# Optimization experiments

Measured on AMD Instinct MI355X. Metric: run time of the kernel, lower is better.

The kernel has to match this reference:

```python
import jax, jax.numpy as jnp
import numpy as np

# dims
L, E, D, DFF, H = 4, 4, 512, 2048, 8
B, T, S, K = 16, 256, 512, 2
HD = D // H


def _ln(x, g, b, eps=1e-5):
    m = x.mean(-1, keepdims=True)
    v = ((x - m) ** 2).mean(-1, keepdims=True)
    return (x - m) / jnp.sqrt(v + eps) * g + b


def _mha(xq, xkv, in_w, in_b, out_w, out_b):
    # torch nn.MultiheadAttention (batch_first), no masks, eval mode
    qw, kw, vw = jnp.split(in_w, 3, axis=0)
    qb, kb, vb = jnp.split(in_b, 3)
    q = xq @ qw.T + qb                       # [B,T,D]
    k = xkv @ kw.T + kb                      # [B,S,D]
    v = xkv @ vw.T + vb
    def heads(t):
        b, s, _ = t.shape
        return t.reshape(b, s, H, HD).transpose(0, 2, 1, 3)
    q, k, v = heads(q), heads(k), heads(v)   # [B,H,*,HD]
    scale = 1.0 / float(np.sqrt(HD))
    a = jax.nn.softmax(jnp.einsum('bhtd,bhsd->bhts', q, k) * scale, axis=-1)
    o = jnp.einsum('bhts,bhsd->bhtd', a, v)
    o = o.transpose(0, 2, 1, 3).reshape(xq.shape[0], xq.shape[1], D)
    return o @ out_w.T + out_b


def _expert(p, x, mem):
    (siw, sib, sow, sob, ciw, cib, cow, cob,
     l1w, l1b, l2w, l2b, g1, b1, g2, b2, g3, b3) = p
    sa = _mha(x, x, siw, sib, sow, sob)
    x = _ln(x + sa, g1, b1)
    ca = _mha(x, mem, ciw, cib, cow, cob)
    x = _ln(x + ca, g2, b2)
    ffn = jax.nn.relu(x @ l1w.T + l1b) @ l2w.T + l2b
    x = _ln(x + ffn, g3, b3)
    return x


def _forward(tgt, memory, router_w, params):
    x = tgt
    for l in range(L):
        pooled = x.mean(axis=1)                      # [B,D] sample-level routing
        logits = pooled @ router_w[l].T              # [B,E]
        vals, idx = jax.lax.top_k(logits, K)
        w = jax.nn.softmax(vals.astype(jnp.float32), axis=-1).astype(x.dtype)
        # dense [B,E] combine weights: zero for unselected experts -> same math
        wf = jnp.zeros((x.shape[0], E), x.dtype).at[jnp.arange(x.shape[0])[:, None], idx].add(w)
        p_l = jax.tree_util.tree_map(lambda a: a[l], params)   # each [E,...]
        outs = jax.vmap(_expert, in_axes=(0, None, None))(p_l, x, memory)  # [E,B,T,D]
        x = jnp.einsum('be,ebtd->btd', wf, outs)
    return x


def setup_inputs() -> dict:
    key = jax.random.key(0)
    ks = jax.random.split(key, 16)
    n = lambda k, shape: jax.random.normal(k, shape, jnp.float32) * 0.02
    return {
        'tgt': jax.random.normal(ks[0], (B, T, D), jnp.float32),
        'memory': jax.random.normal(ks[1], (B, S, D), jnp.float32),
        'router_w': n(ks[2], (L, E, D)),
        'sa_in_w': n(ks[3], (L, E, 3 * D, D)), 'sa_in_b': jnp.zeros((L, E, 3 * D)),
        'sa_out_w': n(ks[4], (L, E, D, D)), 'sa_out_b': jnp.zeros((L, E, D)),
        'ca_in_w': n(ks[5], (L, E, 3 * D, D)), 'ca_in_b': jnp.zeros((L, E, 3 * D)),
        'ca_out_w': n(ks[6], (L, E, D, D)), 'ca_out_b': jnp.zeros((L, E, D)),
        'lin1_w': n(ks[7], (L, E, DFF, D)), 'lin1_b': jnp.zeros((L, E, DFF)),
        'lin2_w': n(ks[8], (L, E, D, DFF)), 'lin2_b': jnp.zeros((L, E, D)),
        'n1_g': jnp.ones((L, E, D)), 'n1_b': jnp.zeros((L, E, D)),
        'n2_g': jnp.ones((L, E, D)), 'n2_b': jnp.zeros((L, E, D)),
        'n3_g': jnp.ones((L, E, D)), 'n3_b': jnp.zeros((L, E, D)),
    }


def reference(tgt, memory, router_w, sa_in_w, sa_in_b, sa_out_w, sa_out_b,
              ca_in_w, ca_in_b, ca_out_w, ca_out_b, lin1_w, lin1_b, lin2_w, lin2_b,
              n1_g, n1_b, n2_g, n2_b, n3_g, n3_b):
    params = (sa_in_w, sa_in_b, sa_out_w, sa_out_b, ca_in_w, ca_in_b, ca_out_w, ca_out_b,
              lin1_w, lin1_b, lin2_w, lin2_b, n1_g, n1_b, n2_g, n2_b, n3_g, n3_b)
    return _forward(tgt, memory, router_w, params)
```

## Files before the change

kernel.cpp:

```cpp
#include <hip/hip_runtime.h>
#include <hip/hip_bf16.h>

#define L_ 4
#define E_ 4
#define D_ 512
#define DFF_ 2048
#define H_ 8
#define B_ 16
#define T_ 256
#define S_ 512
#define HD_ 64
#define NSLOT 32

typedef __attribute__((ext_vector_type(4))) float f32x4;
typedef __attribute__((ext_vector_type(8))) short bf16x8;
typedef __attribute__((ext_vector_type(4))) int i32x4;

static __device__ __forceinline__ float bf2f(unsigned short u){
  union{float f; unsigned u;} c; c.u = ((unsigned)u)<<16; return c.f;
}
static __device__ __forceinline__ unsigned short f2bf(float f){
  union{float f; unsigned u;} c; c.f=f;
  unsigned u=c.u;
  return (unsigned short)((u + 0x7FFFu + ((u>>16)&1u))>>16);
}

static __device__ __forceinline__ void gload16(const unsigned short* g, unsigned short* l){
  __builtin_amdgcn_global_load_lds(
      (const __attribute__((address_space(1))) void*)g,
      (__attribute__((address_space(3))) void*)l, 16, 0, 0);
}

static __device__ __forceinline__ int xcd_swz(int orig, int nwg){
  int q = nwg >> 3, r = nwg & 7;
  int xcd = orig & 7, idx = orig >> 3;
  return (xcd < r) ? (xcd*(q+1) + idx) : (r*(q+1) + (xcd-r)*q + idx);
}

__global__ void __launch_bounds__(256) route_k(const float* __restrict__ x,
    const float* __restrict__ rw, int* __restrict__ eidx, float* __restrict__ wgt)
{
  __shared__ float pooled[D_];
  __shared__ float logit[E_];
  int b = blockIdx.x, tid = threadIdx.x;
  for (int d = tid; d < D_; d += 256) {
    float s = 0.f;
    const float* xp = x + ((long)b*T_)*D_ + d;
    for (int t=0;t<T_;t++) s += xp[(long)t*D_];
    pooled[d] = s * (1.f/T_);
  }
  __syncthreads();
  int wave = tid>>6, lane = tid&63;
  {
    float s=0.f;
    const float* w = rw + (long)wave*D_;
    for (int d=lane; d<D_; d+=64) s += pooled[d]*w[d];
    #pragma unroll
    for (int o=32;o;o>>=1) s += __shfl_xor(s,o);
    if (lane==0) logit[wave] = s;
  }
  __syncthreads();
  if (tid==0){
    int i1=0; float v1=logit[0];
    for (int e=1;e<E_;e++) if (logit[e] > v1){ v1=logit[e]; i1=e; }
    int i2=-1; float v2=-3.4e38f;
    for (int e=0;e<E_;e++) if (e!=i1 && logit[e] > v2){ v2=logit[e]; i2=e; }
    float e2 = __expf(v2 - v1);
    float w1 = 1.f/(1.f+e2);
    eidx[2*b]=i1; eidx[2*b+1]=i2;
    wgt[2*b]=w1; wgt[2*b+1]=e2*w1;
  }
}

__global__ void __launch_bounds__(256) cast_bf16_k(const float* __restrict__ in,
    unsigned short* __restrict__ out, long n){
  long i = ((long)blockIdx.x*blockDim.x + threadIdx.x)*4;
  long st = (long)gridDim.x*blockDim.x*4;
  for (; i<n; i+=st){
    float4 v = *(const float4*)(in+i);
    ushort4 o; o.x=f2bf(v.x); o.y=f2bf(v.y); o.z=f2bf(v.z); o.w=f2bf(v.w);
    *(ushort4*)(out+i) = o;
  }
}

__global__ void __launch_bounds__(256) cast_weights_k(
    const float* __restrict__ s0, const float* __restrict__ s1,
    const float* __restrict__ s2, const float* __restrict__ s3,
    const float* __restrict__ s4, const float* __restrict__ s5,
    unsigned short* __restrict__ d0, unsigned short* __restrict__ d1,
    unsigned short* __restrict__ d2, unsigned short* __restrict__ d3,
    unsigned short* __restrict__ d4, unsigned short* __restrict__ d5)
{
  const long N0=(long)E_*3*D_*D_, N1=(long)E_*D_*D_;
  const long N2=N0, N3=N1, N4=(long)E_*DFF_*D_, N5=N4;
  const long total = N0+N1+N2+N3+N4+N5;
  long i = ((long)blockIdx.x*256 + threadIdx.x)*4;
  long st = (long)gridDim.x*256*4;
  for (; i<total; i+=st){
    const float* s; unsigned short* d; long j = i;
    if (j < N0){ s=s0; d=d0; }
    else if ((j-=N0) < N1){ s=s1; d=d1; }
    else if ((j-=N1) < N2){ s=s2; d=d2; }
    else if ((j-=N2) < N3){ s=s3; d=d3; }
    else if ((j-=N3) < N4){ s=s4; d=d4; }
    else { j-=N4; s=s5; d=d5; }
    float4 v = *(const float4*)(s+j);
    ushort4 o; o.x=f2bf(v.x); o.y=f2bf(v.y); o.z=f2bf(v.z); o.w=f2bf(v.w);
    *(ushort4*)(d+j) = o;
  }
}

__global__ void __launch_bounds__(256) vtrans_k(const unsigned short* __restrict__ src,
    long sSlot, int ld, unsigned short* __restrict__ dst, int rows)
{
  __shared__ unsigned short t[64][68];
  int s0 = blockIdx.x*64; int h = blockIdx.y; int slot = blockIdx.z;
  const unsigned short* sp = src + (long)slot*sSlot + (long)h*64;
  int c = threadIdx.x&63, w = threadIdx.x>>6;
  #pragma unroll
  for (int i=0;i<16;i++){
    int r = i*4 + w;
    t[r][c] = sp[(long)(s0+r)*ld + c];
  }
  __syncthreads();
  unsigned short* dp = dst + ((long)slot*H_ + h)*((long)64*rows) + s0;
  #pragma unroll
  for (int i=0;i<16;i++){
    int d = i*4 + w;
    dp[(long)d*rows + c] = t[c][d];
  }
}

template<int NT>
__global__ void __launch_bounds__(256) fattn_k(
    const unsigned short* __restrict__ Qg, long qSlot, int ldq,
    const unsigned short* __restrict__ Kg, long kSlot, int ldk,
    const unsigned short* __restrict__ Vtg,
    unsigned short* __restrict__ Og, long oSlot, int ldo)
{
  constexpr int SLEN = NT*64;
  __shared__ unsigned short K_lds[64][72];
  __shared__ unsigned short V_lds[64][72];
  __shared__ unsigned short P_lds[4][16][72];

  int nwg = gridDim.x*gridDim.y;
  int wg = xcd_swz(blockIdx.x + gridDim.x*blockIdx.y, nwg);
  int qb = wg % gridDim.x;
  int z  = wg / gridDim.x;
  int slot = z >> 3, h = z & 7;
  int tid = threadIdx.x, wave = tid>>6, lane = tid&63;
  int lr = lane&15, lg = lane>>4;
  int lk = lg*8;

  const unsigned short* Qp = Qg + (long)slot*qSlot + (long)h*HD_;
  const unsigned short* Kp = Kg + (long)slot*kSlot + (long)h*HD_;
  const unsigned short* Vp = Vtg + (long)z*((long)HD_*SLEN);

  bf16x8 qf[2];
  {
    int qrow = qb*64 + wave*16 + lr;
    const unsigned short* qr = Qp + (long)qrow*ldq;
    qf[0] = *(const bf16x8*)(qr + lk);
    qf[1] = *(const bf16x8*)(qr + 32 + lk);
  }

  float m_prev[4], l_run[4];
  f32x4 acc_o[4];
  #pragma unroll
  for (int r=0;r<4;r++){ m_prev[r]=-1e30f; l_run[r]=0.f; }
  #pragma unroll
  for (int ni=0;ni<4;ni++) acc_o[ni]=(f32x4){0.f,0.f,0.f,0.f};

  int srow = tid>>3, sch = tid&7;

  i32x4 kr0 = *(const i32x4*)(Kp + (long)srow*ldk + sch*8);
  i32x4 kr1 = *(const i32x4*)(Kp + (long)(srow+32)*ldk + sch*8);
  i32x4 vr0 = *(const i32x4*)(Vp + (long)srow*SLEN + sch*8);
  i32x4 vr1 = *(const i32x4*)(Vp + (long)(srow+32)*SLEN + sch*8);

  for (int t=0; t<NT; ++t){
    __syncthreads();
    *(i32x4*)&K_lds[srow][sch*8] = kr0;
    *(i32x4*)&K_lds[srow+32][sch*8] = kr1;
    *(i32x4*)&V_lds[srow][sch*8] = vr0;
    *(i32x4*)&V_lds[srow+32][sch*8] = vr1;
    __syncthreads();

    int tn = (t+1 < NT) ? t+1 : t;
    int k0n = tn*64;
    kr0 = *(const i32x4*)(Kp + (long)(k0n+srow)*ldk + sch*8);
    kr1 = *(const i32x4*)(Kp + (long)(k0n+srow+32)*ldk + sch*8);
    vr0 = *(const i32x4*)(Vp + (long)srow*SLEN + k0n + sch*8);
    vr1 = *(const i32x4*)(Vp + (long)(srow+32)*SLEN + k0n + sch*8);

    f32x4 s[4];
    #pragma unroll
    for (int ni=0;ni<4;ni++) s[ni]=(f32x4){0.f,0.f,0.f,0.f};
    __builtin_amdgcn_s_setprio(1);
    #pragma unroll
    for (int ki=0;ki<2;ki++){
      #pragma unroll
      for (int ni=0;ni<4;ni++){
        bf16x8 kf = *(const bf16x8*)&K_lds[ni*16+lr][ki*32+lk];
        s[ni] = __builtin_amdgcn_mfma_f32_16x16x32_bf16(qf[ki], kf, s[ni],0,0,0);
      }
    }
    __builtin_amdgcn_s_setprio(0);
    float tmax[4];
    #pragma unroll
    for (int r=0;r<4;r++){
      tmax[r] = fmaxf(fmaxf(s[0][r],s[1][r]),fmaxf(s[2][r],s[3][r]));
      #pragma unroll
      for (int msk=1; msk<16; msk<<=1) tmax[r]=fmaxf(tmax[r], __shfl_xor(tmax[r],msk));
    }
    bool inc = (tmax[0]>m_prev[0])|(tmax[1]>m_prev[1])|(tmax[2]>m_prev[2])|(tmax[3]>m_prev[3]);
    if (__any(inc)){
      #pragma unroll
      for (int r=0;r<4;r++){
        float mnew = fmaxf(m_prev[r], tmax[r]);
        float corr = __expf(m_prev[r]-mnew);
        m_prev[r] = mnew;
        l_run[r] *= corr;
        #pragma unroll
        for (int ni=0;ni<4;ni++) acc_o[ni][r] *= corr;
      }
    }
    float rs[4] = {0.f,0.f,0.f,0.f};
    #pragma unroll
    for (int ni=0;ni<4;ni++){
      #pragma unroll
      for (int r=0;r<4;r++){
        float p = __expf(s[ni][r]-m_prev[r]);
        rs[r] += p;
        P_lds[wave][lg*4+r][ni*16+lr] = f2bf(p);
      }
    }
    #pragma unroll
    for (int r=0;r<4;r++){
      #pragma unroll
      for (int msk=1; msk<16; msk<<=1) rs[r] += __shfl_xor(rs[r],msk);
      l_run[r] += rs[r];
    }
    __builtin_amdgcn_s_setprio(1);
    #pragma unroll
    for (int ki=0;ki<2;ki++){
      bf16x8 pf = *(const bf16x8*)&P_lds[wave][lr][ki*32+lk];
      #pragma unroll
      for (int ni=0;ni<4;ni++){
        bf16x8 vf = *(const bf16x8*)&V_lds[ni*16+lr][ki*32+lk];
        acc_o[ni] = __builtin_amdgcn_mfma_f32_16x16x32_bf16(pf, vf, acc_o[ni],0,0,0);
      }
    }
    __builtin_amdgcn_s_setprio(0);
  }
  unsigned short* Op = Og + (long)slot*oSlot + (long)h*HD_;
  #pragma unroll
  for (int r=0;r<4;r++){
    float inv = 1.f/l_run[r];
    int q = qb*64 + wave*16 + lg*4 + r;
    #pragma unroll
    for (int ni=0;ni<4;ni++)
      Op[(long)q*ldo + ni*16 + lr] = f2bf(acc_o[ni][r]*inv);
  }
}

template<int BM, int BN, int WTM, int WTN, int BK>
__global__ void __launch_bounds__(512) gemm_lds(
    const unsigned short* __restrict__ A, long aSlot, int aDiv, long aHead, int lda,
    const unsigned short* __restrict__ W, long wSlot, long wHead, long wExp, int ldw,
    const int* __restrict__ eidx, const float* __restrict__ bias, long biasExp,
    void* __restrict__ Cp, long cSlot, long cHead, int ldc,
    int K, int HZ, int f32out, int relu, int scaleNlim, float scaleVal)
{
  constexpr int WAVES_N = BN/WTN;
  constexpr int MI = WTM/16, NI = WTN/16;
  constexpr int SLOTS = BK/8;
  static_assert((BM/WTM)*(BN/WTN) == 8, "8 waves");
  static_assert((BM*SLOTS)%512==0 && (BN*SLOTS)%512==0, "stage coverage");
  __shared__ unsigned short smem[2*(BM+BN)*BK];

  int nwg = gridDim.x*gridDim.y*gridDim.z;
  int wg = xcd_swz(blockIdx.x + gridDim.x*(blockIdx.y + gridDim.y*blockIdx.z), nwg);
  int bx = wg % gridDim.x; int t1 = wg / gridDim.x;
  int by = t1 % gridDim.y; int z  = t1 / gridDim.y;

  int slot = z / HZ;
  int h = z - slot*HZ;
  int e = eidx ? eidx[slot] : 0;
  const unsigned short* Ap = A + (long)(slot/aDiv)*aSlot + (long)h*aHead;
  const unsigned short* Wp = W + (long)slot*wSlot + (long)h*wHead + (long)e*wExp;
  const float* bp = bias ? (bias + (long)e*biasExp) : nullptr;

  int tid  = threadIdx.x;
  int wave = tid>>6, lane = tid&63;
  int wm = wave / WAVES_N, wn = wave % WAVES_N;
  int bm0 = by*BM;
  int bn0 = bx*BN;
  int lr = lane&15;
  int lg = lane>>4;
  int swz = (BK==64) ? (lr&7) : ((lr>>1)&3);

  Ap += (long)bm0*lda;
  Wp += (long)bn0*ldw;

  f32x4 acc[MI][NI];
  #pragma unroll
  for (int i=0;i<MI;i++)
  #pragma unroll
  for (int j=0;j<NI;j++) acc[i][j] = (f32x4){0.f,0.f,0.f,0.f};

  auto stage = [&](int buf, int k0){
    unsigned short* as = &smem[(size_t)buf*(BM+BN)*BK];
    unsigned short* bs = as + BM*BK;
    #pragma unroll
    for (int i=0;i<BM*SLOTS/512;i++){
      int cch = i*512 + tid;
      int row = cch / SLOTS, c = cch % SLOTS;
      int cs = (BK==64) ? (c ^ (row&7)) : (c ^ ((row>>1)&3));
      gload16(Ap + (long)row*lda + k0 + (cs<<3), as + cch*8);
    }
    #pragma unroll
    for (int i=0;i<BN*SLOTS/512;i++){
      int cch = i*512 + tid;
      int row = cch / SLOTS, c = cch % SLOTS;
      int cs = (BK==64) ? (c ^ (row&7)) : (c ^ ((row>>1)&3));
      gload16(Wp + (long)row*ldw + k0 + (cs<<3), bs + cch*8);
    }
  };

  auto compute = [&](int buf){
    unsigned short* as = &smem[(size_t)buf*(BM+BN)*BK];
    unsigned short* bs = as + BM*BK;
    #pragma unroll
    for (int ki=0;ki<BK/32;ki++){
      bf16x8 af[MI], bfr[NI];
      #pragma unroll
      for (int mi=0;mi<MI;mi++){
        int row = wm*WTM + mi*16 + lr;
        af[mi] = *(const bf16x8*)&as[row*BK + (((ki*4+lg) ^ swz)<<3)];
      }
      #pragma unroll
      for (int ni=0;ni<NI;ni++){
        int row = wn*WTN + ni*16 + lr;
        bfr[ni] = *(const bf16x8*)&bs[row*BK + (((ki*4+lg) ^ swz)<<3)];
      }
      __builtin_amdgcn_s_setprio(1);
      #pragma unroll
      for (int mi=0;mi<MI;mi++)
      #pragma unroll
      for (int ni=0;ni<NI;ni++)
        acc[mi][ni] = __builtin_amdgcn_mfma_f32_16x16x32_bf16(af[mi], bfr[ni], acc[mi][ni], 0,0,0);
      __builtin_amdgcn_s_setprio(0);
    }
  };

  int NT = K / BK;
  stage(0, 0);
  __syncthreads();
  int cur = 0;
  for (int t=0; t<NT; ++t){
    if (t+1 < NT) stage(cur^1, (t+1)*BK);
    compute(cur);
    __syncthreads();
    cur ^= 1;
  }

  long cbase = (long)slot*cSlot + (long)h*cHead;
  int rbase = lg*4;
  #pragma unroll
  for (int mi=0;mi<MI;mi++)
  #pragma unroll
  for (int ni=0;ni<NI;ni++){
    f32x4 v = acc[mi][ni];
    int n = bn0 + wn*WTN + ni*16 + lr;
    float bv = bp ? bp[n] : 0.f;
    float scv = (n < scaleNlim) ? scaleVal : 1.f;
    #pragma unroll
    for (int r=0;r<4;r++){
      int m = bm0 + wm*WTM + mi*16 + rbase + r;
      float val = (v[r] + bv) * scv;
      if (relu) val = fmaxf(val, 0.f);
      long o = cbase + (long)m*ldc + n;
      if (f32out) ((float*)Cp)[o] = val;
      else ((unsigned short*)Cp)[o] = f2bf(val);
    }
  }
}

__global__ void __launch_bounds__(256) add_ln_k(
    const float* __restrict__ Ab, int aDiv, long aStride,
    const unsigned short* __restrict__ Bb, long bStride,
    const float* __restrict__ G, const float* __restrict__ Bt,
    const int* __restrict__ eidx,
    float* __restrict__ OutF, unsigned short* __restrict__ OutB)
{
  int row = blockIdx.x*4 + (threadIdx.x>>6);
  int slot = row>>8, t = row&255;
  int lane = threadIdx.x&63;
  const float* a = Ab + (long)(slot/aDiv)*aStride + (long)t*D_;
  const unsigned short* b = Bb + (long)slot*bStride + (long)t*D_;
  int e = eidx[slot];
  const float* g  = G  + (long)e*D_;
  const float* bt = Bt + (long)e*D_;
  float x[8]; float s=0.f;
  #pragma unroll
  for (int i=0;i<8;i++){ x[i] = a[lane+i*64]+bf2f(b[lane+i*64]); s+=x[i]; }
  #pragma unroll
  for (int o=32;o;o>>=1) s += __shfl_xor(s,o);
  float m = s*(1.f/D_);
  float q=0.f;
  #pragma unroll
  for (int i=0;i<8;i++){ float d=x[i]-m; q+=d*d; }
  #pragma unroll
  for (int o=32;o;o>>=1) q += __shfl_xor(q,o);
  float rs = rsqrtf(q*(1.f/D_)+1e-5f);
  long ob = (long)slot*(T_*D_) + (long)t*D_;
  #pragma unroll
  for (int i=0;i<8;i++){
    int d = lane+i*64;
    float y = (x[i]-m)*rs*g[d]+bt[d];
    OutF[ob+d]=y;
    if (OutB) OutB[ob+d]=f2bf(y);
  }
}

__global__ void __launch_bounds__(256) add_ln_comb_k(
    const float* __restrict__ x2, const unsigned short* __restrict__ proj,
    const float* __restrict__ G, const float* __restrict__ Bt,
    const int* __restrict__ eidx, const float* __restrict__ wgt,
    float* __restrict__ dstF, unsigned short* __restrict__ dstB)
{
  int row = blockIdx.x*4 + (threadIdx.x>>6);
  int b = row>>8, t = row&255;
  int lane = threadIdx.x&63;
  float out[8];
  #pragma unroll
  for (int i=0;i<8;i++) out[i]=0.f;
  #pragma unroll
  for (int s2i=0;s2i<2;s2i++){
    int slot = 2*b + s2i;
    int e = eidx[slot];
    float w = wgt[slot];
    const float* a = x2 + (long)slot*(T_*D_) + (long)t*D_;
    const unsigned short* p = proj + (long)slot*(T_*D_) + (long)t*D_;
    const float* g  = G  + (long)e*D_;
    const float* bt = Bt + (long)e*D_;
    float x[8]; float s=0.f;
    #pragma unroll
    for (int i=0;i<8;i++){ x[i] = a[lane+i*64]+bf2f(p[lane+i*64]); s+=x[i]; }
    #pragma unroll
    for (int o=32;o;o>>=1) s += __shfl_xor(s,o);
    float m = s*(1.f/D_);
    float q=0.f;
    #pragma unroll
    for (int i=0;i<8;i++){ float d=x[i]-m; q+=d*d; }
    #pragma unroll
    for (int o=32;o;o>>=1) q += __shfl_xor(q,o);
    float rs = rsqrtf(q*(1.f/D_)+1e-5f);
    #pragma unroll
    for (int i=0;i<8;i++){
      int d = lane+i*64;
      out[i] += w*((x[i]-m)*rs*g[d]+bt[d]);
    }
  }
  long ob = (long)row*D_;
  #pragma unroll
  for (int i=0;i<8;i++){
    int d = lane+i*64;
    dstF[ob+d] = out[i];
    dstB[ob+d] = f2bf(out[i]);
  }
}

extern "C" void kernel_launch(void* const* d_in, const int* in_sizes, int n_in,
                              void* d_out, int out_size, void* d_ws, size_t ws_size,
                              hipStream_t stream)
{
  const float* tgt      = (const float*)d_in[0];
  const float* memory   = (const float*)d_in[1];
  const float* router_w = (const float*)d_in[2];
  const float* sa_in_w  = (const float*)d_in[3];
  const float* sa_in_b  = (const float*)d_in[4];
  const float* sa_out_w = (const float*)d_in[5];
  const float* sa_out_b = (const float*)d_in[6];
  const float* ca_in_w  = (const float*)d_in[7];
  const float* ca_in_b  = (const float*)d_in[8];
  const float* ca_out_w = (const float*)d_in[9];
  const float* ca_out_b = (const float*)d_in[10];
  const float* lin1_w   = (const float*)d_in[11];
  const float* lin1_b   = (const float*)d_in[12];
  const float* lin2_w   = (const float*)d_in[13];
  const float* lin2_b   = (const float*)d_in[14];
  const float* n1_g = (const float*)d_in[15];
  const float* n1_b = (const float*)d_in[16];
  const float* n2_g = (const float*)d_in[17];
  const float* n2_b = (const float*)d_in[18];
  const float* n3_g = (const float*)d_in[19];
  const float* n3_b = (const float*)d_in[20];

  char* ws = (char*)d_ws;
  size_t off = 0;
  auto alloc = [&](size_t bytes)->char*{
    char* p = ws + off; off += (bytes + 255) & ~(size_t)255; return p;
  };
  unsigned short* xb    = (unsigned short*)alloc(2ull*B_*T_*D_);
  unsigned short* memb  = (unsigned short*)alloc(2ull*B_*S_*D_);
  float*          x     = (float*)alloc(4ull*B_*T_*D_);
  int*            eidx  = (int*)alloc(4ull*NSLOT);
  float*          wgt   = (float*)alloc(4ull*NSLOT);
  unsigned short* wSaIn  = (unsigned short*)alloc(2ull*E_*3*D_*D_);
  unsigned short* wSaOut = (unsigned short*)alloc(2ull*E_*D_*D_);
  unsigned short* wCaIn  = (unsigned short*)alloc(2ull*E_*3*D_*D_);
  unsigned short* wCaOut = (unsigned short*)alloc(2ull*E_*D_*D_);
  unsigned short* wL1    = (unsigned short*)alloc(2ull*E_*DFF_*D_);
  unsigned short* wL2    = (unsigned short*)alloc(2ull*E_*D_*DFF_);
  unsigned short* qkv   = (unsigned short*)alloc(2ull*NSLOT*T_*3*D_);
  unsigned short* ffh   = (unsigned short*)alloc(2ull*NSLOT*T_*DFF_);
  unsigned short* attn  = (unsigned short*)alloc(2ull*NSLOT*T_*D_);
  unsigned short* proj  = (unsigned short*)alloc(2ull*NSLOT*T_*D_);
  float*          x1    = (float*)alloc(4ull*NSLOT*T_*D_);
  unsigned short* x1b   = (unsigned short*)alloc(2ull*NSLOT*T_*D_);
  unsigned short* cq    = (unsigned short*)alloc(2ull*NSLOT*T_*D_);
  unsigned short* mkv   = (unsigned short*)alloc(2ull*NSLOT*S_*2*D_);
  float*          x2    = (float*)alloc(4ull*NSLOT*T_*D_);
  unsigned short* x2b   = (unsigned short*)alloc(2ull*NSLOT*T_*D_);
  unsigned short* Vt1   = cq;
  unsigned short* Vt2   = qkv;

  cast_bf16_k<<<1024,256,0,stream>>>(tgt,    xb,   (long)B_*T_*D_);
  cast_bf16_k<<<1024,256,0,stream>>>(memory, memb, (long)B_*S_*D_);

  const float* xcur = tgt;
  for (int l=0; l<L_; ++l){
    route_k<<<B_,256,0,stream>>>(xcur, router_w + (size_t)l*E_*D_, eidx, wgt);
    cast_weights_k<<<2048,256,0,stream>>>(
      sa_in_w  + (size_t)l*E_*3*D_*D_, sa_out_w + (size_t)l*E_*D_*D_,
      ca_in_w  + (size_t)l*E_*3*D_*D_, ca_out_w + (size_t)l*E_*D_*D_,
      lin1_w   + (size_t)l*E_*DFF_*D_, lin2_w   + (size_t)l*E_*D_*DFF_,
      wSaIn, wSaOut, wCaIn, wCaOut, wL1, wL2);

    gemm_lds<128,256,64,64,32><<<dim3(6,2,NSLOT),512,0,stream>>>(
      xb, (long)T_*D_, 2, 0, D_,
      wSaIn, 0, 0, (long)3*D_*D_, D_,
      eidx, sa_in_b + (size_t)l*E_*3*D_, 3*D_,
      qkv, (long)T_*3*D_, 0, 3*D_,
      512, 1, 0, 0, D_, 0.125f);
    vtrans_k<<<dim3(T_/64,H_,NSLOT),256,0,stream>>>(
      qkv + 2*D_, (long)T_*3*D_, 3*D_, Vt1, T_);
    fattn_k<4><<<dim3(T_/64, NSLOT*H_),256,0,stream>>>(
      qkv, (long)T_*3*D_, 3*D_,
      qkv + D_, (long)T_*3*D_, 3*D_,
      Vt1, attn, (long)T_*D_, D_);
    gemm_lds<128,128,64,32,64><<<dim3(4,2,NSLOT),512,0,stream>>>(
      attn, (long)T_*D_, 1, 0, D_,
      wSaOut, 0, 0, (long)D_*D_, D_,
      eidx, sa_out_b + (size_t)l*E_*D_, D_,
      proj, (long)T_*D_, 0, D_,
      512, 1, 0, 0, 0, 1.f);
    add_ln_k<<<2048,256,0,stream>>>(xcur, 2, (long)T_*D_, proj, (long)T_*D_,
      n1_g + (size_t)l*E_*D_, n1_b + (size_t)l*E_*D_, eidx, x1, x1b);
    gemm_lds<128,128,64,32,64><<<dim3(4,2,NSLOT),512,0,stream>>>(
      x1b, (long)T_*D_, 1, 0, D_,
      wCaIn, 0, 0, (long)3*D_*D_, D_,
      eidx, ca_in_b + (size_t)l*E_*3*D_, 3*D_,
      cq, (long)T_*D_, 0, D_,
      512, 1, 0, 0, D_, 0.125f);
    gemm_lds<128,256,64,64,32><<<dim3(4,4,NSLOT),512,0,stream>>>(
      memb, (long)S_*D_, 2, 0, D_,
      wCaIn + (size_t)D_*D_, 0, 0, (long)3*D_*D_, D_,
      eidx, ca_in_b + (size_t)l*E_*3*D_ + D_, 3*D_,
      mkv, (long)S_*2*D_, 0, 2*D_,
      512, 1, 0, 0, 0, 1.f);
    vtrans_k<<<dim3(S_/64,H_,NSLOT),256,0,stream>>>(
      mkv + D_, (long)S_*2*D_, 2*D_, Vt2, S_);
    fattn_k<8><<<dim3(T_/64, NSLOT*H_),256,0,stream>>>(
      cq, (long)T_*D_, D_,
      mkv, (long)S_*2*D_, 2*D_,
      Vt2, attn, (long)T_*D_, D_);
    gemm_lds<128,128,64,32,64><<<dim3(4,2,NSLOT),512,0,stream>>>(
      attn, (long)T_*D_, 1, 0, D_,
      wCaOut, 0, 0, (long)D_*D_, D_,
      eidx, ca_out_b + (size_t)l*E_*D_, D_,
      proj, (long)T_*D_, 0, D_,
      512, 1, 0, 0, 0, 1.f);
    add_ln_k<<<2048,256,0,stream>>>(x1, 1, (long)T_*D_, proj, (long)T_*D_,
      n2_g + (size_t)l*E_*D_, n2_b + (size_t)l*E_*D_, eidx, x2, x2b);
    gemm_lds<128,256,64,64,32><<<dim3(8,2,NSLOT),512,0,stream>>>(
      x2b, (long)T_*D_, 1, 0, D_,
      wL1, 0, 0, (long)DFF_*D_, D_,
      eidx, lin1_b + (size_t)l*E_*DFF_, DFF_,
      ffh, (long)T_*DFF_, 0, DFF_,
      512, 1, 0, 1, 0, 1.f);
    gemm_lds<128,128,64,32,64><<<dim3(4,2,NSLOT),512,0,stream>>>(
      ffh, (long)T_*DFF_, 1, 0, DFF_,
      wL2, 0, 0, (long)D_*DFF_, DFF_,
      eidx, lin2_b + (size_t)l*E_*D_, D_,
      proj, (long)T_*D_, 0, D_,
      2048, 1, 0, 0, 0, 1.f);
    float* dstF = (l==L_-1) ? (float*)d_out : x;
    add_ln_comb_k<<<1024,256,0,stream>>>(x2, proj,
      n3_g + (size_t)l*E_*D_, n3_b + (size_t)l*E_*D_, eidx, wgt, dstF, xb);
    xcur = x;
  }
}
```

Before: 1.081 ms.

## Parallelize routing pool, drop fp32 residual copies, vectorize layernorm kernels

```diff
diff --git a/kernel.cpp b/kernel.cpp
--- a/kernel.cpp
+++ b/kernel.cpp
@@ -37,16 +37,32 @@
   return (xcd < r) ? (xcd*(q+1) + idx) : (r*(q+1) + (xcd-r)*q + idx);
 }
 
-__global__ void __launch_bounds__(256) route_k(const float* __restrict__ x,
+__global__ void __launch_bounds__(256) pool_k(const float* __restrict__ x,
+    float* __restrict__ part)
+{
+  int b = blockIdx.x >> 3, ch = blockIdx.x & 7;
+  int tid = threadIdx.x;
+  const float* xp = x + ((long)b*T_ + ch*32)*D_ + tid*2;
+  float s0=0.f, s1=0.f;
+  #pragma unroll 8
+  for (int t=0;t<32;t++){
+    float2 v = *(const float2*)(xp + (long)t*D_);
+    s0 += v.x; s1 += v.y;
+  }
+  float* pp = part + ((long)b*8 + ch)*D_ + tid*2;
+  pp[0]=s0; pp[1]=s1;
+}
+
+__global__ void __launch_bounds__(256) route2_k(const float* __restrict__ part,
     const float* __restrict__ rw, int* __restrict__ eidx, float* __restrict__ wgt)
 {
   __shared__ float pooled[D_];
   __shared__ float logit[E_];
   int b = blockIdx.x, tid = threadIdx.x;
-  for (int d = tid; d < D_; d += 256) {
+  for (int d = tid; d < D_; d += 256){
     float s = 0.f;
-    const float* xp = x + ((long)b*T_)*D_ + d;
-    for (int t=0;t<T_;t++) s += xp[(long)t*D_];
+    #pragma unroll
+    for (int c=0;c<8;c++) s += part[((long)b*8 + c)*D_ + d];
     pooled[d] = s * (1.f/T_);
   }
   __syncthreads();
@@ -387,24 +403,37 @@
   }
 }
 
+template<int ABF>
 __global__ void __launch_bounds__(256) add_ln_k(
-    const float* __restrict__ Ab, int aDiv, long aStride,
+    const void* __restrict__ Ab_, int aDiv, long aStride,
     const unsigned short* __restrict__ Bb, long bStride,
     const float* __restrict__ G, const float* __restrict__ Bt,
     const int* __restrict__ eidx,
-    float* __restrict__ OutF, unsigned short* __restrict__ OutB)
+    unsigned short* __restrict__ OutB)
 {
   int row = blockIdx.x*4 + (threadIdx.x>>6);
   int slot = row>>8, t = row&255;
   int lane = threadIdx.x&63;
-  const float* a = Ab + (long)(slot/aDiv)*aStride + (long)t*D_;
-  const unsigned short* b = Bb + (long)slot*bStride + (long)t*D_;
-  int e = eidx[slot];
-  const float* g  = G  + (long)e*D_;
-  const float* bt = Bt + (long)e*D_;
-  float x[8]; float s=0.f;
-  #pragma unroll
-  for (int i=0;i<8;i++){ x[i] = a[lane+i*64]+bf2f(b[lane+i*64]); s+=x[i]; }
+  int d0 = lane*8;
+  float x[8];
+  if (ABF){
+    const unsigned short* a = (const unsigned short*)Ab_ + (long)(slot/aDiv)*aStride + (long)t*D_ + d0;
+    ushort4 a0 = *(const ushort4*)a, a1 = *(const ushort4*)(a+4);
+    x[0]=bf2f(a0.x); x[1]=bf2f(a0.y); x[2]=bf2f(a0.z); x[3]=bf2f(a0.w);
+    x[4]=bf2f(a1.x); x[5]=bf2f(a1.y); x[6]=bf2f(a1.z); x[7]=bf2f(a1.w);
+  } else {
+    const float* a = (const float*)Ab_ + (long)(slot/aDiv)*aStride + (long)t*D_ + d0;
+    float4 a0 = *(const float4*)a, a1 = *(const float4*)(a+4);
+    x[0]=a0.x; x[1]=a0.y; x[2]=a0.z; x[3]=a0.w;
+    x[4]=a1.x; x[5]=a1.y; x[6]=a1.z; x[7]=a1.w;
+  }
+  const unsigned short* b = Bb + (long)slot*bStride + (long)t*D_ + d0;
+  ushort4 b0 = *(const ushort4*)b, b1 = *(const ushort4*)(b+4);
+  x[0]+=bf2f(b0.x); x[1]+=bf2f(b0.y); x[2]+=bf2f(b0.z); x[3]+=bf2f(b0.w);
+  x[4]+=bf2f(b1.x); x[5]+=bf2f(b1.y); x[6]+=bf2f(b1.z); x[7]+=bf2f(b1.w);
+  float s=0.f;
+  #pragma unroll
+  for (int i=0;i<8;i++) s += x[i];
   #pragma unroll
   for (int o=32;o;o>>=1) s += __shfl_xor(s,o);
   float m = s*(1.f/D_);
@@ -414,18 +443,27 @@
   #pragma unroll
   for (int o=32;o;o>>=1) q += __shfl_xor(q,o);
   float rs = rsqrtf(q*(1.f/D_)+1e-5f);
-  long ob = (long)slot*(T_*D_) + (long)t*D_;
-  #pragma unroll
-  for (int i=0;i<8;i++){
-    int d = lane+i*64;
-    float y = (x[i]-m)*rs*g[d]+bt[d];
-    OutF[ob+d]=y;
-    if (OutB) OutB[ob+d]=f2bf(y);
-  }
+  int e = eidx[slot];
+  const float* g  = G  + (long)e*D_ + d0;
+  const float* bt = Bt + (long)e*D_ + d0;
+  float4 g0 = *(const float4*)g, g1 = *(const float4*)(g+4);
+  float4 t0 = *(const float4*)bt, t1 = *(const float4*)(bt+4);
+  float gg[8] = {g0.x,g0.y,g0.z,g0.w,g1.x,g1.y,g1.z,g1.w};
+  float tt[8] = {t0.x,t0.y,t0.z,t0.w,t1.x,t1.y,t1.z,t1.w};
+  long ob = (long)slot*(T_*D_) + (long)t*D_ + d0;
+  ushort4 o0, o1;
+  float y0=(x[0]-m)*rs*gg[0]+tt[0], y1=(x[1]-m)*rs*gg[1]+tt[1];
+  float y2=(x[2]-m)*rs*gg[2]+tt[2], y3=(x[3]-m)*rs*gg[3]+tt[3];
+  float y4=(x[4]-m)*rs*gg[4]+tt[4], y5=(x[5]-m)*rs*gg[5]+tt[5];
+  float y6=(x[6]-m)*rs*gg[6]+tt[6], y7=(x[7]-m)*rs*gg[7]+tt[7];
+  o0.x=f2bf(y0); o0.y=f2bf(y1); o0.z=f2bf(y2); o0.w=f2bf(y3);
+  o1.x=f2bf(y4); o1.y=f2bf(y5); o1.z=f2bf(y6); o1.w=f2bf(y7);
+  *(ushort4*)(OutB+ob) = o0;
+  *(ushort4*)(OutB+ob+4) = o1;
 }
 
 __global__ void __launch_bounds__(256) add_ln_comb_k(
-    const float* __restrict__ x2, const unsigned short* __restrict__ proj,
+    const unsigned short* __restrict__ x2b, const unsigned short* __restrict__ proj,
     const float* __restrict__ G, const float* __restrict__ Bt,
     const int* __restrict__ eidx, const float* __restrict__ wgt,
     float* __restrict__ dstF, unsigned short* __restrict__ dstB)
@@ -433,6 +471,7 @@
   int row = blockIdx.x*4 + (threadIdx.x>>6);
   int b = row>>8, t = row&255;
   int lane = threadIdx.x&63;
+  int d0 = lane*8;
   float out[8];
   #pragma unroll
   for (int i=0;i<8;i++) out[i]=0.f;
@@ -441,13 +480,18 @@
     int slot = 2*b + s2i;
     int e = eidx[slot];
     float w = wgt[slot];
-    const float* a = x2 + (long)slot*(T_*D_) + (long)t*D_;
-    const unsigned short* p = proj + (long)slot*(T_*D_) + (long)t*D_;
-    const float* g  = G  + (long)e*D_;
-    const float* bt = Bt + (long)e*D_;
-    float x[8]; float s=0.f;
-    #pragma unroll
-    for (int i=0;i<8;i++){ x[i] = a[lane+i*64]+bf2f(p[lane+i*64]); s+=x[i]; }
+    const unsigned short* a = x2b + (long)slot*(T_*D_) + (long)t*D_ + d0;
+    const unsigned short* p = proj + (long)slot*(T_*D_) + (long)t*D_ + d0;
+    ushort4 a0 = *(const ushort4*)a, a1 = *(const ushort4*)(a+4);
+    ushort4 p0 = *(const ushort4*)p, p1 = *(const ushort4*)(p+4);
+    float x[8];
+    x[0]=bf2f(a0.x)+bf2f(p0.x); x[1]=bf2f(a0.y)+bf2f(p0.y);
+    x[2]=bf2f(a0.z)+bf2f(p0.z); x[3]=bf2f(a0.w)+bf2f(p0.w);
+    x[4]=bf2f(a1.x)+bf2f(p1.x); x[5]=bf2f(a1.y)+bf2f(p1.y);
+    x[6]=bf2f(a1.z)+bf2f(p1.z); x[7]=bf2f(a1.w)+bf2f(p1.w);
+    float s=0.f;
+    #pragma unroll
+    for (int i=0;i<8;i++) s += x[i];
     #pragma unroll
     for (int o=32;o;o>>=1) s += __shfl_xor(s,o);
     float m = s*(1.f/D_);
@@ -457,19 +501,25 @@
     #pragma unroll
     for (int o=32;o;o>>=1) q += __shfl_xor(q,o);
     float rs = rsqrtf(q*(1.f/D_)+1e-5f);
-    #pragma unroll
-    for (int i=0;i<8;i++){
-      int d = lane+i*64;
-      out[i] += w*((x[i]-m)*rs*g[d]+bt[d]);
-    }
-  }
-  long ob = (long)row*D_;
-  #pragma unroll
-  for (int i=0;i<8;i++){
-    int d = lane+i*64;
-    dstF[ob+d] = out[i];
-    dstB[ob+d] = f2bf(out[i]);
-  }
+    const float* g  = G  + (long)e*D_ + d0;
+    const float* bt = Bt + (long)e*D_ + d0;
+    float4 g0 = *(const float4*)g, g1 = *(const float4*)(g+4);
+    float4 t0 = *(const float4*)bt, t1 = *(const float4*)(bt+4);
+    float gg[8] = {g0.x,g0.y,g0.z,g0.w,g1.x,g1.y,g1.z,g1.w};
+    float tt[8] = {t0.x,t0.y,t0.z,t0.w,t1.x,t1.y,t1.z,t1.w};
+    #pragma unroll
+    for (int i=0;i<8;i++) out[i] += w*((x[i]-m)*rs*gg[i]+tt[i]);
+  }
+  long ob = (long)row*D_ + d0;
+  float4 f0 = {out[0],out[1],out[2],out[3]};
+  float4 f1 = {out[4],out[5],out[6],out[7]};
+  *(float4*)(dstF+ob) = f0;
+  *(float4*)(dstF+ob+4) = f1;
+  ushort4 o0, o1;
+  o0.x=f2bf(out[0]); o0.y=f2bf(out[1]); o0.z=f2bf(out[2]); o0.w=f2bf(out[3]);
+  o1.x=f2bf(out[4]); o1.y=f2bf(out[5]); o1.z=f2bf(out[6]); o1.w=f2bf(out[7]);
+  *(ushort4*)(dstB+ob) = o0;
+  *(ushort4*)(dstB+ob+4) = o1;
 }
 
 extern "C" void kernel_launch(void* const* d_in, const int* in_sizes, int n_in,
@@ -506,6 +556,7 @@
   unsigned short* xb    = (unsigned short*)alloc(2ull*B_*T_*D_);
   unsigned short* memb  = (unsigned short*)alloc(2ull*B_*S_*D_);
   float*          x     = (float*)alloc(4ull*B_*T_*D_);
+  float*          part  = (float*)alloc(4ull*B_*8*D_);
   int*            eidx  = (int*)alloc(4ull*NSLOT);
   float*          wgt   = (float*)alloc(4ull*NSLOT);
   unsigned short* wSaIn  = (unsigned short*)alloc(2ull*E_*3*D_*D_);
@@ -518,11 +569,9 @@
   unsigned short* ffh   = (unsigned short*)alloc(2ull*NSLOT*T_*DFF_);
   unsigned short* attn  = (unsigned short*)alloc(2ull*NSLOT*T_*D_);
   unsigned short* proj  = (unsigned short*)alloc(2ull*NSLOT*T_*D_);
-  float*          x1    = (float*)alloc(4ull*NSLOT*T_*D_);
   unsigned short* x1b   = (unsigned short*)alloc(2ull*NSLOT*T_*D_);
   unsigned short* cq    = (unsigned short*)alloc(2ull*NSLOT*T_*D_);
   unsigned short* mkv   = (unsigned short*)alloc(2ull*NSLOT*S_*2*D_);
-  float*          x2    = (float*)alloc(4ull*NSLOT*T_*D_);
   unsigned short* x2b   = (unsigned short*)alloc(2ull*NSLOT*T_*D_);
   unsigned short* Vt1   = cq;
   unsigned short* Vt2   = qkv;
@@ -532,7 +581,8 @@
 
   const float* xcur = tgt;
   for (int l=0; l<L_; ++l){
-    route_k<<<B_,256,0,stream>>>(xcur, router_w + (size_t)l*E_*D_, eidx, wgt);
+    pool_k<<<B_*8,256,0,stream>>>(xcur, part);
+    route2_k<<<B_,256,0,stream>>>(part, router_w + (size_t)l*E_*D_, eidx, wgt);
     cast_weights_k<<<2048,256,0,stream>>>(
       sa_in_w  + (size_t)l*E_*3*D_*D_, sa_out_w + (size_t)l*E_*D_*D_,
       ca_in_w  + (size_t)l*E_*3*D_*D_, ca_out_w + (size_t)l*E_*D_*D_,
@@ -557,8 +607,8 @@
       eidx, sa_out_b + (size_t)l*E_*D_, D_,
       proj, (long)T_*D_, 0, D_,
       512, 1, 0, 0, 0, 1.f);
-    add_ln_k<<<2048,256,0,stream>>>(xcur, 2, (long)T_*D_, proj, (long)T_*D_,
-      n1_g + (size_t)l*E_*D_, n1_b + (size_t)l*E_*D_, eidx, x1, x1b);
+    add_ln_k<0><<<2048,256,0,stream>>>(xcur, 2, (long)T_*D_, proj, (long)T_*D_,
+      n1_g + (size_t)l*E_*D_, n1_b + (size_t)l*E_*D_, eidx, x1b);
     gemm_lds<128,128,64,32,64><<<dim3(4,2,NSLOT),512,0,stream>>>(
       x1b, (long)T_*D_, 1, 0, D_,
       wCaIn, 0, 0, (long)3*D_*D_, D_,
@@ -583,8 +633,8 @@
       eidx, ca_out_b + (size_t)l*E_*D_, D_,
       proj, (long)T_*D_, 0, D_,
       512, 1, 0, 0, 0, 1.f);
-    add_ln_k<<<2048,256,0,stream>>>(x1, 1, (long)T_*D_, proj, (long)T_*D_,
-      n2_g + (size_t)l*E_*D_, n2_b + (size_t)l*E_*D_, eidx, x2, x2b);
+    add_ln_k<1><<<2048,256,0,stream>>>(x1b, 1, (long)T_*D_, proj, (long)T_*D_,
+      n2_g + (size_t)l*E_*D_, n2_b + (size_t)l*E_*D_, eidx, x2b);
     gemm_lds<128,256,64,64,32><<<dim3(8,2,NSLOT),512,0,stream>>>(
       x2b, (long)T_*D_, 1, 0, D_,
       wL1, 0, 0, (long)DFF_*D_, D_,
@@ -598,7 +648,7 @@
       proj, (long)T_*D_, 0, D_,
       2048, 1, 0, 0, 0, 1.f);
     float* dstF = (l==L_-1) ? (float*)d_out : x;
-    add_ln_comb_k<<<1024,256,0,stream>>>(x2, proj,
+    add_ln_comb_k<<<1024,256,0,stream>>>(x2b, proj,
       n3_g + (size_t)l*E_*D_, n3_b + (size_t)l*E_*D_, eidx, wgt, dstF, xb);
     xcur = x;
   }
```

Result: faster. 986.2 us (-8.8%).
